# Optimization experiments

Hardware: AMD Instinct MI355X
Metric: run time of the kernel (lower is better)

## Reference

```python
import jax, jax.numpy as jnp
import numpy as np

K = 7            # involution kernel size
GC = 16          # group_channels (canonical involution)
EPS = 1e-6


def ln_cf(x, w, b):
    # channels_first LayerNorm over channel dim (axis=1), as in ConvNeXt utils
    u = jnp.mean(x, axis=1, keepdims=True)
    s = jnp.mean((x - u) ** 2, axis=1, keepdims=True)
    xn = (x - u) / jnp.sqrt(s + EPS)
    return w[:, None, None] * xn + b[:, None, None]


def gelu(x):
    return jax.nn.gelu(x, approximate=False)  # torch nn.GELU default (erf)


def involution(x, w1, b1, w2, b2):
    # x: (B,C,H,W). Kernel-generating head: 1x1 conv -> ReLU -> 1x1 conv.
    B, C, H, W = x.shape
    G = C // GC
    mid = jnp.einsum('bchw,mc->bmhw', x, w1) + b1[None, :, None, None]
    mid = jax.nn.relu(mid)
    wk = jnp.einsum('bmhw,km->bkhw', mid, w2) + b2[None, :, None, None]
    wk = wk.reshape(B, G, K * K, H, W)  # per-pixel, per-group K*K kernels
    pad = (K - 1) // 2
    xp = jnp.pad(x, ((0, 0), (0, 0), (pad, pad), (pad, pad)))
    out = jnp.zeros((B, G, GC, H, W), dtype=x.dtype)
    # accumulate over the K*K spatial offsets (fixed small loop, no big unfold)
    for idx in range(K * K):
        i, j = divmod(idx, K)
        xs = xp[:, :, i:i + H, j:j + W].reshape(B, G, GC, H, W)
        out = out + wk[:, :, idx][:, :, None] * xs
    return out.reshape(B, C, H, W)


def setup_inputs() -> dict:
    key = jax.random.key(0)
    ks = jax.random.split(key, 8)
    B, C, O, H, Wd = 4, 128, 256, 128, 128
    mid = C // 4
    G = C // GC
    sc = 0.05
    return {
        'x': jax.random.normal(ks[0], (B, C, H, Wd), jnp.float32),
        'w1': jax.random.normal(ks[1], (mid, C), jnp.float32) * sc,
        'b1': jnp.zeros((mid,), jnp.float32),
        'w2': jax.random.normal(ks[2], (K * K * G, mid), jnp.float32) * sc,
        'b2': jnp.zeros((K * K * G,), jnp.float32),
        'ln1_w': jnp.ones((C,), jnp.float32),
        'ln1_b': jnp.zeros((C,), jnp.float32),
        'conv_w': jax.random.normal(ks[3], (O, C), jnp.float32) * sc,
        'ln2_w': jnp.ones((O,), jnp.float32),
        'ln2_b': jnp.zeros((O,), jnp.float32),
        'map_w': jax.random.normal(ks[4], (O, C), jnp.float32) * sc,
        'map_b': jnp.zeros((O,), jnp.float32),
        'ln3_w': jnp.ones((O,), jnp.float32),
        'ln3_b': jnp.zeros((O,), jnp.float32),
    }


def reference(x, w1, b1, w2, b2, ln1_w, ln1_b, conv_w, ln2_w, ln2_b,
              map_w, map_b, ln3_w, ln3_b):
    # invblock: Involution -> LayerNorm(channels_first) -> GELU
    x1 = involution(x, w1, b1, w2, b2)
    x1 = gelu(ln_cf(x1, ln1_w, ln1_b))
    # conv_block: 1x1 conv (no bias) -> LayerNorm
    x1 = ln_cf(jnp.einsum('bchw,oc->bohw', x1, conv_w), ln2_w, ln2_b)
    # mapping (channels differ): 1x1 conv (bias) -> LayerNorm
    xm = jnp.einsum('bchw,oc->bohw', x, map_w) + map_b[None, :, None, None]
    xm = ln_cf(xm, ln3_w, ln3_b)
    return gelu(x1 + xm)
```

## Files before the change

### kernel.cpp

```cpp
#include <hip/hip_runtime.h>

typedef unsigned short ushort_t;
typedef unsigned int uint_t;

#define NB 4
#define NC 128
#define NH 128
#define NW 128
#define NPIX 65536
#define NMID 32
#define NKK 49
#define NK 392
#define NKP 400
#define NO 256
#define LN_EPS 1e-6f

typedef __attribute__((ext_vector_type(8))) short short8;
typedef __attribute__((ext_vector_type(4))) float floatx4;

__device__ __forceinline__ float bf2f(ushort_t u) {
    union { uint_t i; float f; } v; v.i = ((uint_t)u) << 16; return v.f;
}
__device__ __forceinline__ float bf2f_lo(uint_t u) {
    union { uint_t i; float f; } v; v.i = u << 16; return v.f;
}
__device__ __forceinline__ float bf2f_hi(uint_t u) {
    union { uint_t i; float f; } v; v.i = u & 0xffff0000u; return v.f;
}
__device__ __forceinline__ ushort_t f2bf(float f) {
    union { float f; uint_t i; } v; v.f = f;
    uint_t x = v.i;
    uint_t r = (x + 0x7FFFu + ((x >> 16) & 1u)) >> 16;
    return (ushort_t)r;
}
__device__ __forceinline__ float gelu_f(float x) {
    return 0.5f * x * (1.0f + erff(x * 0.70710678118654752f));
}
__device__ __forceinline__ float ldin(const void* p, int i, int isf32) {
    return isf32 ? ((const float*)p)[i] : bf2f(((const ushort_t*)p)[i]);
}
__device__ __forceinline__ void gload_lds16(const void* g, void* l) {
    __builtin_amdgcn_global_load_lds(
        (const __attribute__((address_space(1))) void*)g,
        (__attribute__((address_space(3))) void*)l, 16, 0, 0);
}

__global__ void kdetect(const uint_t* __restrict__ xw, int* __restrict__ flag) {
    int lane = threadIdx.x;
    int cnt = 0;
    for (int j = 0; j < 8; j++) {
        uint_t w = xw[lane * 8 + j];
        uint_t e = (w >> 7) & 0xffu;
        if (e >= 110u && e <= 135u) cnt++;
    }
    for (int d = 1; d < 64; d <<= 1) cnt += __shfl_xor(cnt, d);
    if (lane == 0) flag[0] = (cnt < 256) ? 1 : 0;
}

__global__ void ksentinel(uint_t* __restrict__ out, int nwords) {
    int i = blockIdx.x * 256 + threadIdx.x;
    if (i < nwords) out[i] = 0x40004000u;
}

__global__ __launch_bounds__(256) void ktrans(const void* __restrict__ x,
                                              ushort_t* __restrict__ xT,
                                              const int* __restrict__ flag) {
    int isf32 = flag[0];
    int b = blockIdx.z, h = blockIdx.y;
    int wchunk = blockIdx.x & 1, cchunk = blockIdx.x >> 1;
    int w0 = wchunk << 6, c0 = cchunk << 5;
    __shared__ ushort_t tile[32][66];
    int tx = threadIdx.x & 63, ty = threadIdx.x >> 6;
    for (int r = 0; r < 32; r += 4) {
        int idx = (((b * NC + c0 + r + ty) * NH) + h) * NW + w0 + tx;
        tile[r + ty][tx] = isf32 ? f2bf(((const float*)x)[idx])
                                 : ((const ushort_t*)x)[idx];
    }
    __syncthreads();
    int cc = threadIdx.x & 31, wq = threadIdx.x >> 5;
    for (int pp = 0; pp < 64; pp += 8) {
        int wx = pp + wq;
        xT[((size_t)((b * NH + h) * NW) + w0 + wx) * NC + c0 + cc] = tile[cc][wx];
    }
}

__global__ __launch_bounds__(256) void kprep(const void* w1, const void* w2,
                                             const void* b1, const void* b2,
                                             const void* ln1w, const void* ln1b,
                                             const void* ln2w, const void* ln2b,
                                             const void* map_b,
                                             const void* ln3w, const void* ln3b,
                                             const int* __restrict__ flag,
                                             ushort_t* __restrict__ w1b,
                                             ushort_t* __restrict__ w2b,
                                             float* __restrict__ b1f,
                                             float* __restrict__ b2f,
                                             float* __restrict__ ln1wf,
                                             float* __restrict__ ln1bf,
                                             float* __restrict__ ln2wf,
                                             float* __restrict__ ln2bf,
                                             float* __restrict__ mbf,
                                             float* __restrict__ ln3wf,
                                             float* __restrict__ ln3bf) {
    int isf32 = flag[0];
    int i = blockIdx.x * 256 + threadIdx.x;
    if (i < NMID * NC) w1b[i] = f2bf(ldin(w1, i, isf32));
    if (i < NKP * NMID) w2b[i] = (i < NK * NMID) ? f2bf(ldin(w2, i, isf32))
                                                 : (ushort_t)0;
    if (i < NMID) b1f[i] = ldin(b1, i, isf32);
    if (i < NKP)  b2f[i] = (i < NK) ? ldin(b2, i, isf32) : 0.f;
    if (i < NC) { ln1wf[i] = ldin(ln1w, i, isf32); ln1bf[i] = ldin(ln1b, i, isf32); }
    if (i < NO) {
        ln2wf[i] = ldin(ln2w, i, isf32); ln2bf[i] = ldin(ln2b, i, isf32);
        mbf[i]   = ldin(map_b, i, isf32);
        ln3wf[i] = ldin(ln3w, i, isf32); ln3bf[i] = ldin(ln3b, i, isf32);
    }
}

__global__ __launch_bounds__(256) void kfrag(const void* conv_w, const void* map_w,
                                             const int* __restrict__ flag,
                                             ushort_t* __restrict__ wfrag) {
    int isf32 = flag[0];
    int cid = blockIdx.x * 256 + threadIdx.x;
    int lane = cid & 63, n4 = (cid >> 6) & 15, br = (cid >> 10) & 1, kb = cid >> 11;
    int o = n4 * 16 + (lane & 15);
    int ch0 = kb * 32 + (lane >> 4) * 8;
    const void* src = br ? map_w : conv_w;
    ushort_t* dst = wfrag + (size_t)cid * 8;
#pragma unroll
    for (int j = 0; j < 8; j++)
        dst[j] = f2bf(ldin(src, o * NC + ch0 + j, isf32));
}

__global__ __launch_bounds__(256) void k1a(const ushort_t* __restrict__ xT,
                                           const ushort_t* __restrict__ w1b,
                                           const float* __restrict__ b1f,
                                           const ushort_t* __restrict__ w2b,
                                           const float* __restrict__ b2f,
                                           ushort_t* __restrict__ wkT) {
    __shared__ ushort_t midbuf[64 * 32];
    __shared__ ushort_t wkstage[NKP * 66];

    int t = threadIdx.x;
    int lane = t & 63;
    int w = __builtin_amdgcn_readfirstlane(t >> 6);
    int l16 = lane & 15, quad = lane >> 4;
    int tileid = blockIdx.x;
    int tilex = tileid & 15, tiley = (tileid >> 4) & 15, b = tileid >> 8;
    int h0 = tiley * 8, w0 = tilex * 8;

    int lpx_a = 16 * w + l16;
    int py = lpx_a >> 3, pxx = lpx_a & 7;
    const ushort_t* abase = xT + (size_t)((b * NH + h0 + py) * NW + w0 + pxx) * NC + quad * 8;
    floatx4 am0 = (floatx4)0.f, am1 = (floatx4)0.f;
#pragma unroll
    for (int kb = 0; kb < 4; kb++) {
        short8 a   = *(const short8*)(abase + kb * 32);
        short8 b0  = *(const short8*)(w1b + (l16) * NC + kb * 32 + quad * 8);
        short8 b1v = *(const short8*)(w1b + (16 + l16) * NC + kb * 32 + quad * 8);
        am0 = __builtin_amdgcn_mfma_f32_16x16x32_bf16(a, b0, am0, 0, 0, 0);
        am1 = __builtin_amdgcn_mfma_f32_16x16x32_bf16(a, b1v, am1, 0, 0, 0);
    }
    {
        float bia0 = b1f[l16], bia1 = b1f[16 + l16];
#pragma unroll
        for (int r = 0; r < 4; r++) {
            int m = 16 * w + quad * 4 + r;
            midbuf[m * 32 + l16]      = f2bf(fmaxf(am0[r] + bia0, 0.f));
            midbuf[m * 32 + 16 + l16] = f2bf(fmaxf(am1[r] + bia1, 0.f));
        }
    }
    __syncthreads();

    short8 aM = *(const short8*)(midbuf + (16 * w + l16) * 32 + quad * 8);
#pragma unroll
    for (int nt = 0; nt < 25; nt++) {
        int n = nt * 16 + l16;
        short8 bw = *(const short8*)(w2b + n * 32 + quad * 8);
        floatx4 c = __builtin_amdgcn_mfma_f32_16x16x32_bf16(aM, bw, (floatx4)0.f, 0, 0, 0);
        float bias = b2f[n];
#pragma unroll
        for (int r = 0; r < 4; r++)
            wkstage[n * 66 + 16 * w + quad * 4 + r] = f2bf(c[r] + bias);
    }
    __syncthreads();

    int krow = t >> 5, px2 = t & 31;
    for (int it = 0; it < 50; it++) {
        int k = it * 8 + krow;
        uint_t v = *(const uint_t*)&wkstage[k * 66 + 2 * px2];
        *(uint_t*)&wkT[(size_t)k * NPIX + tileid * 64 + 2 * px2] = v;
    }
}

__global__ __launch_bounds__(512) void k1b(const ushort_t* __restrict__ xT,
                                           const ushort_t* __restrict__ wkT,
                                           const float* __restrict__ ln1wf,
                                           const float* __restrict__ ln1bf,
                                           ushort_t* __restrict__ y1) {
    __shared__ __align__(16) char smem[50432];
    uint4* x8   = (uint4*)smem;
    float* sred = (float*)smem;

    int t = threadIdx.x;
    int lane = t & 63;
    int w = __builtin_amdgcn_readfirstlane(t >> 6);
    int tileid = blockIdx.x;
    int tilex = tileid & 15, tiley = (tileid >> 4) & 15, b = tileid >> 8;
    int h0 = tiley * 8, w0 = tilex * 8;
    int py = lane >> 3, pxx = lane & 7;

    const ushort_t* wkbase = wkT + (size_t)(w * NKK) * NPIX + tileid * 64 + lane;
    uint_t wkp[25];
#pragma unroll
    for (int j = 0; j < 24; j++) {
        uint_t lo = wkbase[(size_t)(2 * j) * NPIX];
        uint_t hi = wkbase[(size_t)(2 * j + 1) * NPIX];
        wkp[j] = lo | (hi << 16);
    }
    wkp[24] = wkbase[(size_t)48 * NPIX];

    for (int it = 0; it < 7; it++) {
        int idx = it * 512 + t;
        if (idx < 3136) {
            int oct = idx & 15, hp = idx >> 4;
            int hy = hp / 14, hx = hp - hy * 14;
            int gh = h0 + hy - 3, gw = w0 + hx - 3;
            uint4 v = make_uint4(0u, 0u, 0u, 0u);
            if ((unsigned)gh < (unsigned)NH && (unsigned)gw < (unsigned)NW) {
                v = *(const uint4*)&xT[(size_t)((b * NH + gh) * NW + gw) * NC + 8 * oct];
            }
            x8[oct * 197 + hp] = v;
        }
    }
    __syncthreads();

    int base0 = py * 14 + pxx;
    float a[16];
#pragma unroll
    for (int j = 0; j < 16; j++) a[j] = 0.f;

#pragma unroll
    for (int tap = 0; tap < NKK; tap++) {
        float wkf = (tap & 1) ? bf2f((ushort_t)(wkp[tap >> 1] >> 16))
                              : bf2f((ushort_t)(wkp[tap >> 1] & 0xffffu));
        int xa = base0 + (tap / 7) * 14 + (tap % 7);
        uint4 u0 = x8[(2 * w) * 197 + xa];
        uint4 u1 = x8[(2 * w + 1) * 197 + xa];
        a[0]  = fmaf(wkf, bf2f_lo(u0.x), a[0]);
        a[1]  = fmaf(wkf, bf2f_hi(u0.x), a[1]);
        a[2]  = fmaf(wkf, bf2f_lo(u0.y), a[2]);
        a[3]  = fmaf(wkf, bf2f_hi(u0.y), a[3]);
        a[4]  = fmaf(wkf, bf2f_lo(u0.z), a[4]);
        a[5]  = fmaf(wkf, bf2f_hi(u0.z), a[5]);
        a[6]  = fmaf(wkf, bf2f_lo(u0.w), a[6]);
        a[7]  = fmaf(wkf, bf2f_hi(u0.w), a[7]);
        a[8]  = fmaf(wkf, bf2f_lo(u1.x), a[8]);
        a[9]  = fmaf(wkf, bf2f_hi(u1.x), a[9]);
        a[10] = fmaf(wkf, bf2f_lo(u1.y), a[10]);
        a[11] = fmaf(wkf, bf2f_hi(u1.y), a[11]);
        a[12] = fmaf(wkf, bf2f_lo(u1.z), a[12]);
        a[13] = fmaf(wkf, bf2f_hi(u1.z), a[13]);
        a[14] = fmaf(wkf, bf2f_lo(u1.w), a[14]);
        a[15] = fmaf(wkf, bf2f_hi(u1.w), a[15]);
    }
    __syncthreads();

    float s = 0.f, sq = 0.f;
#pragma unroll
    for (int j = 0; j < 16; j++) { s += a[j]; sq += a[j] * a[j]; }
    sred[(w * 64 + lane) * 2]     = s;
    sred[(w * 64 + lane) * 2 + 1] = sq;
    __syncthreads();
    float ts = 0.f, tq = 0.f;
#pragma unroll
    for (int r = 0; r < 8; r++) {
        ts += sred[(r * 64 + lane) * 2];
        tq += sred[(r * 64 + lane) * 2 + 1];
    }
    float mean = ts * (1.0f / NC);
    float var = tq * (1.0f / NC) - mean * mean;
    float rstd = rsqrtf(var + LN_EPS);

    int p = (b * NH + h0 + py) * NW + w0 + pxx;
    uint_t pk[8];
#pragma unroll
    for (int j = 0; j < 8; j++) {
        int c0 = 16 * w + 2 * j;
        float g0 = gelu_f((a[2 * j] - mean) * rstd * ln1wf[c0] + ln1bf[c0]);
        float g1 = gelu_f((a[2 * j + 1] - mean) * rstd * ln1wf[c0 + 1] + ln1bf[c0 + 1]);
        pk[j] = (uint_t)f2bf(g0) | ((uint_t)f2bf(g1) << 16);
    }
    uint4* dst = (uint4*)(y1 + (size_t)p * NC + 16 * w);
    dst[0] = make_uint4(pk[0], pk[1], pk[2], pk[3]);
    dst[1] = make_uint4(pk[4], pk[5], pk[6], pk[7]);
}

__global__ __launch_bounds__(64) void k1_fused(const ushort_t* __restrict__ xT,
                                               const ushort_t* __restrict__ w1b,
                                               const float* __restrict__ b1f,
                                               const ushort_t* __restrict__ w2b,
                                               const float* __restrict__ b2f,
                                               const float* __restrict__ ln1wf,
                                               const float* __restrict__ ln1bf,
                                               ushort_t* __restrict__ y1) {
    __shared__ ushort_t midbuf[16 * 32];
    __shared__ ushort_t wkbuf[16 * NKP];

    int lane = threadIdx.x;
    int l16 = lane & 15, quad = lane >> 4;
    int b = blockIdx.z;
    int h0 = blockIdx.y * 2, w0 = blockIdx.x * 8;

    int Pa = (b * NH + h0 + (l16 >> 3)) * NW + w0 + (l16 & 7);
    const ushort_t* abase = xT + (size_t)Pa * NC + quad * 8;
    floatx4 am0 = (floatx4)0.f, am1 = (floatx4)0.f;
#pragma unroll
    for (int kb = 0; kb < 4; kb++) {
        short8 a   = *(const short8*)(abase + kb * 32);
        short8 b0  = *(const short8*)(w1b + (l16) * NC + kb * 32 + quad * 8);
        short8 b1v = *(const short8*)(w1b + (16 + l16) * NC + kb * 32 + quad * 8);
        am0 = __builtin_amdgcn_mfma_f32_16x16x32_bf16(a, b0, am0, 0, 0, 0);
        am1 = __builtin_amdgcn_mfma_f32_16x16x32_bf16(a, b1v, am1, 0, 0, 0);
    }
    {
        float bia0 = b1f[l16], bia1 = b1f[16 + l16];
#pragma unroll
        for (int r = 0; r < 4; r++) {
            int m = quad * 4 + r;
            midbuf[m * 32 + l16]      = f2bf(fmaxf(am0[r] + bia0, 0.f));
            midbuf[m * 32 + 16 + l16] = f2bf(fmaxf(am1[r] + bia1, 0.f));
        }
    }
    __syncthreads();

    short8 aM = *(const short8*)(midbuf + l16 * 32 + quad * 8);
#pragma unroll
    for (int nt = 0; nt < 25; nt++) {
        int n = nt * 16 + l16;
        short8 bw = *(const short8*)(w2b + n * 32 + quad * 8);
        floatx4 c = __builtin_amdgcn_mfma_f32_16x16x32_bf16(aM, bw, (floatx4)0.f, 0, 0, 0);
        float bias = b2f[n];
#pragma unroll
        for (int r = 0; r < 4; r++)
            wkbuf[(quad * 4 + r) * NKP + n] = f2bf(c[r] + bias);
    }
    __syncthreads();

    int g = lane >> 3;
    float l1w0 = ln1wf[2 * lane], l1w1 = ln1wf[2 * lane + 1];
    float l1b0 = ln1bf[2 * lane], l1b1 = ln1bf[2 * lane + 1];

    for (int i = 0; i < 16; i++) {
        int hh0 = h0 + (i >> 3), ww0 = w0 + (i & 7);
        int p = (b * NH + hh0) * NW + ww0;
        const ushort_t* wkrow = wkbuf + i * NKP + g * NKK;
        float a0 = 0.f, a1 = 0.f;
#pragma unroll
        for (int dy = -3; dy <= 3; dy++) {
            int hh = hh0 + dy;
            if ((unsigned)hh >= (unsigned)NH) continue;
#pragma unroll
            for (int dx = -3; dx <= 3; dx++) {
                int ww = ww0 + dx;
                if ((unsigned)ww >= (unsigned)NW) continue;
                float wkv = bf2f(wkrow[(dy + 3) * 7 + (dx + 3)]);
                uint_t xp = *(const uint_t*)(xT + ((size_t)(p + dy * NW + dx)) * NC + 2 * lane);
                a0 = fmaf(wkv, bf2f((ushort_t)(xp & 0xffffu)), a0);
                a1 = fmaf(wkv, bf2f((ushort_t)(xp >> 16)), a1);
            }
        }
        float s = a0 + a1, sq = a0 * a0 + a1 * a1;
#pragma unroll
        for (int d = 1; d < 64; d <<= 1) {
            s  += __shfl_xor(s, d);
            sq += __shfl_xor(sq, d);
        }
        float mean = s * (1.0f / NC);
        float var = sq * (1.0f / NC) - mean * mean;
        float rstd = rsqrtf(var + LN_EPS);
        float g0 = gelu_f((a0 - mean) * rstd * l1w0 + l1b0);
        float g1 = gelu_f((a1 - mean) * rstd * l1w1 + l1b1);
        uint_t pk = (uint_t)f2bf(g0) | ((uint_t)f2bf(g1) << 16);
        *(uint_t*)(y1 + (size_t)p * NC + 2 * lane) = pk;
    }
}

__global__ __launch_bounds__(256, 2) void k23(const ushort_t* __restrict__ y1,
                                              const ushort_t* __restrict__ xT,
                                              const ushort_t* __restrict__ wfrag,
                                              const float* __restrict__ mbf,
                                              const float* __restrict__ ln2wf,
                                              const float* __restrict__ ln2bf,
                                              const float* __restrict__ ln3wf,
                                              const float* __restrict__ ln3bf,
                                              void* __restrict__ out,
                                              const int* __restrict__ flag) {
    __shared__ __align__(16) char sbuf[65536];

    int isf32 = flag[0];
    int t = threadIdx.x;
    int lane = t & 63;
    int w = __builtin_amdgcn_readfirstlane(t >> 6);
    int quad = lane >> 4, l16 = lane & 15;

    int P0 = blockIdx.x * 64;
    int pw = P0 + w * 16;
    const ushort_t* aYp = y1 + (size_t)(pw + l16) * NC + quad * 8;
    const ushort_t* aXp = xT + (size_t)(pw + l16) * NC + quad * 8;

    {
        const ushort_t* gsrc = wfrag + (size_t)(w * 512 + lane) * 8;
        char* ldst = sbuf + (size_t)(w * 512) * 16;
#pragma unroll
        for (int i = 0; i < 8; i++)
            gload_lds16(gsrc + i * 64 * 8, ldst + i * 64 * 16);
    }
    short8 aYr[4], aXr[4];
#pragma unroll
    for (int kb = 0; kb < 4; kb++) {
        aYr[kb] = *(const short8*)(aYp + kb * 32);
        aXr[kb] = *(const short8*)(aXp + kb * 32);
    }
    __syncthreads();

    floatx4 accC[16], accM[16];
#pragma unroll
    for (int n4 = 0; n4 < 16; n4++) { accC[n4] = (floatx4)0.f; accM[n4] = (floatx4)0.f; }

#pragma unroll
    for (int kb = 0; kb < 4; kb++) {
        const char* bufr = sbuf + (kb & 1) * 32768;
        if (kb < 3) {
            char* bufw = sbuf + ((kb + 1) & 1) * 32768;
            const ushort_t* gsrc = wfrag + ((size_t)(kb + 1) * 2048 + w * 512 + lane) * 8;
            char* ldst = bufw + (size_t)(w * 512) * 16;
#pragma unroll
            for (int i = 0; i < 8; i++)
                gload_lds16(gsrc + i * 64 * 8, ldst + i * 64 * 16);
        }
        short8 aY = aYr[kb], aX = aXr[kb];
#pragma unroll
        for (int n4 = 0; n4 < 16; n4++) {
            short8 bc = *(const short8*)(bufr + (size_t)(n4 * 64 + lane) * 16);
            short8 bm = *(const short8*)(bufr + (size_t)(1024 + n4 * 64 + lane) * 16);
            accC[n4] = __builtin_amdgcn_mfma_f32_16x16x32_bf16(aY, bc, accC[n4], 0, 0, 0);
            accM[n4] = __builtin_amdgcn_mfma_f32_16x16x32_bf16(aX, bm, accM[n4], 0, 0, 0);
        }
        if (kb < 3) __syncthreads();
    }

#pragma unroll
    for (int n4 = 0; n4 < 16; n4++) {
        float mb = mbf[n4 * 16 + l16];
#pragma unroll
        for (int r = 0; r < 4; r++) accM[n4][r] += mb;
    }

    floatx4 s1 = (floatx4)0.f, q1 = (floatx4)0.f, s2 = (floatx4)0.f, q2 = (floatx4)0.f;
#pragma unroll
    for (int n4 = 0; n4 < 16; n4++)
#pragma unroll
        for (int r = 0; r < 4; r++) {
            float a = accC[n4][r], m = accM[n4][r];
            s1[r] += a; q1[r] += a * a;
            s2[r] += m; q2[r] += m * m;
        }
#pragma unroll
    for (int d = 1; d < 16; d <<= 1) {
#pragma unroll
        for (int r = 0; r < 4; r++) {
            s1[r] += __shfl_xor(s1[r], d);
            q1[r] += __shfl_xor(q1[r], d);
            s2[r] += __shfl_xor(s2[r], d);
            q2[r] += __shfl_xor(q2[r], d);
        }
    }
    floatx4 m1, r1, m2, r2;
#pragma unroll
    for (int r = 0; r < 4; r++) {
        m1[r] = s1[r] * (1.0f / NO);
        r1[r] = rsqrtf(q1[r] * (1.0f / NO) - m1[r] * m1[r] + LN_EPS);
        m2[r] = s2[r] * (1.0f / NO);
        r2[r] = rsqrtf(q2[r] * (1.0f / NO) - m2[r] * m2[r] + LN_EPS);
    }

    int batch = pw >> 14;
    int plocal = (pw & 16383) + quad * 4;
#pragma unroll
    for (int n4 = 0; n4 < 16; n4++) {
        int o = n4 * 16 + l16;
        float l2w = ln2wf[o], l2b = ln2bf[o];
        float l3w = ln3wf[o], l3b = ln3bf[o];
        float4 gv;
        {
            float v1, v2;
            v1 = (accC[n4][0] - m1[0]) * r1[0] * l2w + l2b;
            v2 = (accM[n4][0] - m2[0]) * r2[0] * l3w + l3b;
            gv.x = gelu_f(v1 + v2);
            v1 = (accC[n4][1] - m1[1]) * r1[1] * l2w + l2b;
            v2 = (accM[n4][1] - m2[1]) * r2[1] * l3w + l3b;
            gv.y = gelu_f(v1 + v2);
            v1 = (accC[n4][2] - m1[2]) * r1[2] * l2w + l2b;
            v2 = (accM[n4][2] - m2[2]) * r2[2] * l3w + l3b;
            gv.z = gelu_f(v1 + v2);
            v1 = (accC[n4][3] - m1[3]) * r1[3] * l2w + l2b;
            v2 = (accM[n4][3] - m2[3]) * r2[3] * l3w + l3b;
            gv.w = gelu_f(v1 + v2);
        }
        size_t oi = ((size_t)(batch * NO + o) << 14) + plocal;
        if (isf32) {
            *(float4*)((float*)out + oi) = gv;
        } else {
            uint_t p0 = (uint_t)f2bf(gv.x) | ((uint_t)f2bf(gv.y) << 16);
            uint_t p1 = (uint_t)f2bf(gv.z) | ((uint_t)f2bf(gv.w) << 16);
            *(uint2*)((ushort_t*)out + oi) = make_uint2(p0, p1);
        }
    }
}

extern "C" void kernel_launch(void* const* d_in, const int* in_sizes, int n_in,
                              void* d_out, int out_size, void* d_ws, size_t ws_size,
                              hipStream_t stream) {
    const void* x      = d_in[0];
    const void* w1     = d_in[1];
    const void* b1     = d_in[2];
    const void* w2     = d_in[3];
    const void* b2     = d_in[4];
    const void* ln1w   = d_in[5];
    const void* ln1b   = d_in[6];
    const void* conv_w = d_in[7];
    const void* ln2w   = d_in[8];
    const void* ln2b   = d_in[9];
    const void* map_w  = d_in[10];
    const void* map_b  = d_in[11];
    const void* ln3w   = d_in[12];
    const void* ln3b   = d_in[13];

    char* ws = (char*)d_ws;
    ushort_t* xT    = (ushort_t*)(ws);
    ushort_t* y1    = (ushort_t*)(ws + 16777216);
    ushort_t* wfrag = (ushort_t*)(ws + 33554432);
    ushort_t* w1b   = (ushort_t*)(ws + 33685504);
    ushort_t* w2b   = (ushort_t*)(ws + 33693696);
    float*    b1f   = (float*)(ws + 33719296);
    float*    b2f   = (float*)(ws + 33719424);
    float*    ln1wf = (float*)(ws + 33721024);
    float*    ln1bf = (float*)(ws + 33721536);
    float*    mbf   = (float*)(ws + 33722048);
    float*    ln2wf = (float*)(ws + 33723072);
    float*    ln2bf = (float*)(ws + 33724096);
    float*    ln3wf = (float*)(ws + 33725120);
    float*    ln3bf = (float*)(ws + 33726144);
    int*      flag  = (int*)(ws + 33727168);
    const size_t NEED_SMALL = 33727184;
    ushort_t* wkT   = (ushort_t*)(ws + 33727232);
    const size_t NEED_BIG = 33727232 + (size_t)NKP * NPIX * 2;

    if (ws_size < NEED_SMALL) {
        int nwords = out_size / 2;
        ksentinel<<<(nwords + 255) / 256, 256, 0, stream>>>((uint_t*)d_out, nwords);
        return;
    }

    kdetect<<<1, 64, 0, stream>>>((const uint_t*)x, flag);
    kprep<<<128, 256, 0, stream>>>(w1, w2, b1, b2, ln1w, ln1b,
                                   ln2w, ln2b, map_b, ln3w, ln3b, flag,
                                   w1b, w2b, b1f, b2f, ln1wf, ln1bf,
                                   ln2wf, ln2bf, mbf, ln3wf, ln3bf);
    kfrag<<<32, 256, 0, stream>>>(conv_w, map_w, flag, wfrag);
    ktrans<<<dim3(8, 128, 4), 256, 0, stream>>>(x, xT, flag);

    if (ws_size >= NEED_BIG) {
        k1a<<<1024, 256, 0, stream>>>(xT, w1b, b1f, w2b, b2f, wkT);
        k1b<<<1024, 512, 0, stream>>>(xT, wkT, ln1wf, ln1bf, y1);
    } else {
        k1_fused<<<dim3(16, 64, 4), 64, 0, stream>>>(xT, w1b, b1f, w2b, b2f,
                                                     ln1wf, ln1bf, y1);
    }

    k23<<<NPIX / 64, 256, 0, stream>>>(y1, xT, wfrag, mbf,
                                       ln2wf, ln2bf, ln3wf, ln3bf, d_out, flag);
}
```

Before: 229.9 us.

## Split k23 conv and mapping GEMMs across wave pairs to raise occupancy

k23 now pairs waves: one wave of each pair computes the conv GEMM plus LN2 for 16 pixels, the other computes the mapping GEMM plus LN3. The two halves are exchanged through shared memory before the final add and GELU. Each wave keeps half the accumulators, LDS drops to 32KB with single buffering, launch bounds go to 4 blocks per CU, and the grid doubles to 32 pixels per block. This is meant to cut register and LDS pressure and raise occupancy. The cost is losing the double-buffered weight prefetch, which adds an extra barrier per k-step, plus an extra LDS exchange.

```diff
diff --git a/kernel.cpp b/kernel.cpp
--- a/kernel.cpp
+++ b/kernel.cpp
@@ -386,7 +386,7 @@
     }
 }
 
-__global__ __launch_bounds__(256, 2) void k23(const ushort_t* __restrict__ y1,
+__global__ __launch_bounds__(256, 4) void k23(const ushort_t* __restrict__ y1,
                                               const ushort_t* __restrict__ xT,
                                               const ushort_t* __restrict__ wfrag,
                                               const float* __restrict__ mbf,
@@ -396,18 +396,19 @@
                                               const float* __restrict__ ln3bf,
                                               void* __restrict__ out,
                                               const int* __restrict__ flag) {
-    __shared__ __align__(16) char sbuf[65536];
+    __shared__ __align__(16) char sbuf[32768];
 
     int isf32 = flag[0];
     int t = threadIdx.x;
     int lane = t & 63;
     int w = __builtin_amdgcn_readfirstlane(t >> 6);
     int quad = lane >> 4, l16 = lane & 15;
-
-    int P0 = blockIdx.x * 64;
-    int pw = P0 + w * 16;
-    const ushort_t* aYp = y1 + (size_t)(pw + l16) * NC + quad * 8;
-    const ushort_t* aXp = xT + (size_t)(pw + l16) * NC + quad * 8;
+    int pair = w >> 1;
+    int isM  = w & 1;
+
+    int P0 = blockIdx.x * 32;
+    int pw = P0 + pair * 16;
+    const ushort_t* Abase = (isM ? xT : y1) + (size_t)(pw + l16) * NC + quad * 8;
 
     {
         const ushort_t* gsrc = wfrag + (size_t)(w * 512 + lane) * 8;
@@ -416,104 +417,110 @@
         for (int i = 0; i < 8; i++)
             gload_lds16(gsrc + i * 64 * 8, ldst + i * 64 * 16);
     }
-    short8 aYr[4], aXr[4];
+    short8 Ar[4];
+#pragma unroll
+    for (int kb = 0; kb < 4; kb++) Ar[kb] = *(const short8*)(Abase + kb * 32);
+
+    __syncthreads();
+
+    floatx4 acc[16];
+#pragma unroll
+    for (int n4 = 0; n4 < 16; n4++) acc[n4] = (floatx4)0.f;
+
+    const char* bbase = sbuf + isM * 16384;
 #pragma unroll
     for (int kb = 0; kb < 4; kb++) {
-        aYr[kb] = *(const short8*)(aYp + kb * 32);
-        aXr[kb] = *(const short8*)(aXp + kb * 32);
-    }
-    __syncthreads();
-
-    floatx4 accC[16], accM[16];
-#pragma unroll
-    for (int n4 = 0; n4 < 16; n4++) { accC[n4] = (floatx4)0.f; accM[n4] = (floatx4)0.f; }
-
-#pragma unroll
-    for (int kb = 0; kb < 4; kb++) {
-        const char* bufr = sbuf + (kb & 1) * 32768;
+        short8 a = Ar[kb];
+#pragma unroll
+        for (int n4 = 0; n4 < 16; n4++) {
+            short8 b = *(const short8*)(bbase + (size_t)(n4 * 64 + lane) * 16);
+            acc[n4] = __builtin_amdgcn_mfma_f32_16x16x32_bf16(a, b, acc[n4], 0, 0, 0);
+        }
+        __syncthreads();
         if (kb < 3) {
-            char* bufw = sbuf + ((kb + 1) & 1) * 32768;
             const ushort_t* gsrc = wfrag + ((size_t)(kb + 1) * 2048 + w * 512 + lane) * 8;
-            char* ldst = bufw + (size_t)(w * 512) * 16;
+            char* ldst = sbuf + (size_t)(w * 512) * 16;
 #pragma unroll
             for (int i = 0; i < 8; i++)
                 gload_lds16(gsrc + i * 64 * 8, ldst + i * 64 * 16);
-        }
-        short8 aY = aYr[kb], aX = aXr[kb];
+            __syncthreads();
+        }
+    }
+
+    if (isM) {
 #pragma unroll
         for (int n4 = 0; n4 < 16; n4++) {
-            short8 bc = *(const short8*)(bufr + (size_t)(n4 * 64 + lane) * 16);
-            short8 bm = *(const short8*)(bufr + (size_t)(1024 + n4 * 64 + lane) * 16);
-            accC[n4] = __builtin_amdgcn_mfma_f32_16x16x32_bf16(aY, bc, accC[n4], 0, 0, 0);
-            accM[n4] = __builtin_amdgcn_mfma_f32_16x16x32_bf16(aX, bm, accM[n4], 0, 0, 0);
-        }
-        if (kb < 3) __syncthreads();
-    }
-
+            float mb = mbf[n4 * 16 + l16];
+#pragma unroll
+            for (int r = 0; r < 4; r++) acc[n4][r] += mb;
+        }
+    }
+
+    floatx4 s = (floatx4)0.f, q = (floatx4)0.f;
+#pragma unroll
+    for (int n4 = 0; n4 < 16; n4++)
+#pragma unroll
+        for (int r = 0; r < 4; r++) {
+            float a = acc[n4][r];
+            s[r] += a; q[r] += a * a;
+        }
+#pragma unroll
+    for (int d = 1; d < 16; d <<= 1) {
+#pragma unroll
+        for (int r = 0; r < 4; r++) {
+            s[r] += __shfl_xor(s[r], d);
+            q[r] += __shfl_xor(q[r], d);
+        }
+    }
+    floatx4 mn, rs;
+#pragma unroll
+    for (int r = 0; r < 4; r++) {
+        mn[r] = s[r] * (1.0f / NO);
+        rs[r] = rsqrtf(q[r] * (1.0f / NO) - mn[r] * mn[r] + LN_EPS);
+    }
+
+    const float* lnw = isM ? ln3wf : ln2wf;
+    const float* lnb = isM ? ln3bf : ln2bf;
 #pragma unroll
     for (int n4 = 0; n4 < 16; n4++) {
-        float mb = mbf[n4 * 16 + l16];
-#pragma unroll
-        for (int r = 0; r < 4; r++) accM[n4][r] += mb;
-    }
-
-    floatx4 s1 = (floatx4)0.f, q1 = (floatx4)0.f, s2 = (floatx4)0.f, q2 = (floatx4)0.f;
-#pragma unroll
-    for (int n4 = 0; n4 < 16; n4++)
-#pragma unroll
-        for (int r = 0; r < 4; r++) {
-            float a = accC[n4][r], m = accM[n4][r];
-            s1[r] += a; q1[r] += a * a;
-            s2[r] += m; q2[r] += m * m;
-        }
-#pragma unroll
-    for (int d = 1; d < 16; d <<= 1) {
-#pragma unroll
-        for (int r = 0; r < 4; r++) {
-            s1[r] += __shfl_xor(s1[r], d);
-            q1[r] += __shfl_xor(q1[r], d);
-            s2[r] += __shfl_xor(s2[r], d);
-            q2[r] += __shfl_xor(q2[r], d);
-        }
-    }
-    floatx4 m1, r1, m2, r2;
-#pragma unroll
-    for (int r = 0; r < 4; r++) {
-        m1[r] = s1[r] * (1.0f / NO);
-        r1[r] = rsqrtf(q1[r] * (1.0f / NO) - m1[r] * m1[r] + LN_EPS);
-        m2[r] = s2[r] * (1.0f / NO);
-        r2[r] = rsqrtf(q2[r] * (1.0f / NO) - m2[r] * m2[r] + LN_EPS);
-    }
-
+        int o = n4 * 16 + l16;
+        float ww = lnw[o], bb = lnb[o];
+#pragma unroll
+        for (int r = 0; r < 4; r++)
+            acc[n4][r] = (acc[n4][r] - mn[r]) * rs[r] * ww + bb;
+    }
+
+    float* preg = (float*)(sbuf + pair * 16384);
+    if (!isM) {
+#pragma unroll
+        for (int j = 0; j < 8; j++)
+            *(floatx4*)(preg + j * 256 + lane * 4) = acc[8 + j];
+    } else {
+#pragma unroll
+        for (int j = 0; j < 8; j++)
+            *(floatx4*)(preg + 2048 + j * 256 + lane * 4) = acc[j];
+    }
+    __syncthreads();
+
+    int n4base = isM ? 8 : 0;
+    const float* rdp = preg + (isM ? 0 : 2048);
     int batch = pw >> 14;
     int plocal = (pw & 16383) + quad * 4;
 #pragma unroll
-    for (int n4 = 0; n4 < 16; n4++) {
+    for (int j = 0; j < 8; j++) {
+        int n4 = n4base + j;
+        floatx4 other = *(const floatx4*)(rdp + j * 256 + lane * 4);
+        float g0 = gelu_f(acc[n4][0] + other[0]);
+        float g1 = gelu_f(acc[n4][1] + other[1]);
+        float g2 = gelu_f(acc[n4][2] + other[2]);
+        float g3 = gelu_f(acc[n4][3] + other[3]);
         int o = n4 * 16 + l16;
-        float l2w = ln2wf[o], l2b = ln2bf[o];
-        float l3w = ln3wf[o], l3b = ln3bf[o];
-        float4 gv;
-        {
-            float v1, v2;
-            v1 = (accC[n4][0] - m1[0]) * r1[0] * l2w + l2b;
-            v2 = (accM[n4][0] - m2[0]) * r2[0] * l3w + l3b;
-            gv.x = gelu_f(v1 + v2);
-            v1 = (accC[n4][1] - m1[1]) * r1[1] * l2w + l2b;
-            v2 = (accM[n4][1] - m2[1]) * r2[1] * l3w + l3b;
-            gv.y = gelu_f(v1 + v2);
-            v1 = (accC[n4][2] - m1[2]) * r1[2] * l2w + l2b;
-            v2 = (accM[n4][2] - m2[2]) * r2[2] * l3w + l3b;
-            gv.z = gelu_f(v1 + v2);
-            v1 = (accC[n4][3] - m1[3]) * r1[3] * l2w + l2b;
-            v2 = (accM[n4][3] - m2[3]) * r2[3] * l3w + l3b;
-            gv.w = gelu_f(v1 + v2);
-        }
         size_t oi = ((size_t)(batch * NO + o) << 14) + plocal;
         if (isf32) {
-            *(float4*)((float*)out + oi) = gv;
+            *(float4*)((float*)out + oi) = make_float4(g0, g1, g2, g3);
         } else {
-            uint_t p0 = (uint_t)f2bf(gv.x) | ((uint_t)f2bf(gv.y) << 16);
-            uint_t p1 = (uint_t)f2bf(gv.z) | ((uint_t)f2bf(gv.w) << 16);
+            uint_t p0 = (uint_t)f2bf(g0) | ((uint_t)f2bf(g1) << 16);
+            uint_t p1 = (uint_t)f2bf(g2) | ((uint_t)f2bf(g3) << 16);
             *(uint2*)((ushort_t*)out + oi) = make_uint2(p0, p1);
         }
     }
@@ -579,6 +586,6 @@
                                                      ln1wf, ln1bf, y1);
     }
 
-    k23<<<NPIX / 64, 256, 0, stream>>>(y1, xT, wfrag, mbf,
+    k23<<<NPIX / 32, 256, 0, stream>>>(y1, xT, wfrag, mbf,
                                        ln2wf, ln2bf, ln3wf, ln3bf, d_out, flag);
 }
```

Result: slower. 331.8 us (+44.4%).

## Split k23 output channels across wave pairs and single-buffer weight LDS

Applied to the files above, without the earlier changes.

Each 16-pixel tile in k23 is now shared by two waves, and each wave computes half of the 256 output channels. The two halves' LayerNorm partial sums are combined through shared memory. This halves the accumulator registers per wave. The weight staging buffer goes from double to single buffering (32KB), and launch bounds rise to 3 blocks per CU. The aim is higher occupancy and more blocks, in exchange for losing the overlap of weight loads with MFMA, adding extra barriers, and loading each A fragment redundantly in both waves of a pair.

```diff
diff --git a/kernel.cpp b/kernel.cpp
--- a/kernel.cpp
+++ b/kernel.cpp
@@ -386,7 +386,7 @@
     }
 }
 
-__global__ __launch_bounds__(256, 2) void k23(const ushort_t* __restrict__ y1,
+__global__ __launch_bounds__(256, 3) void k23(const ushort_t* __restrict__ y1,
                                               const ushort_t* __restrict__ xT,
                                               const ushort_t* __restrict__ wfrag,
                                               const float* __restrict__ mbf,
@@ -396,16 +396,18 @@
                                               const float* __restrict__ ln3bf,
                                               void* __restrict__ out,
                                               const int* __restrict__ flag) {
-    __shared__ __align__(16) char sbuf[65536];
+    __shared__ __align__(16) char sbuf[32768];
 
     int isf32 = flag[0];
     int t = threadIdx.x;
     int lane = t & 63;
     int w = __builtin_amdgcn_readfirstlane(t >> 6);
     int quad = lane >> 4, l16 = lane & 15;
-
-    int P0 = blockIdx.x * 64;
-    int pw = P0 + w * 16;
+    int pair = w >> 1;
+    int oh   = w & 1;
+
+    int P0 = blockIdx.x * 32;
+    int pw = P0 + pair * 16;
     const ushort_t* aYp = y1 + (size_t)(pw + l16) * NC + quad * 8;
     const ushort_t* aXp = xT + (size_t)(pw + l16) * NC + quad * 8;
 
@@ -416,53 +418,53 @@
         for (int i = 0; i < 8; i++)
             gload_lds16(gsrc + i * 64 * 8, ldst + i * 64 * 16);
     }
-    short8 aYr[4], aXr[4];
+    short8 Ay[4], Ax[4];
 #pragma unroll
     for (int kb = 0; kb < 4; kb++) {
-        aYr[kb] = *(const short8*)(aYp + kb * 32);
-        aXr[kb] = *(const short8*)(aXp + kb * 32);
-    }
-    __syncthreads();
-
-    floatx4 accC[16], accM[16];
-#pragma unroll
-    for (int n4 = 0; n4 < 16; n4++) { accC[n4] = (floatx4)0.f; accM[n4] = (floatx4)0.f; }
+        Ay[kb] = *(const short8*)(aYp + kb * 32);
+        Ax[kb] = *(const short8*)(aXp + kb * 32);
+    }
+    __syncthreads();
+
+    floatx4 accC[8], accM[8];
+#pragma unroll
+    for (int j = 0; j < 8; j++) { accC[j] = (floatx4)0.f; accM[j] = (floatx4)0.f; }
 
 #pragma unroll
     for (int kb = 0; kb < 4; kb++) {
-        const char* bufr = sbuf + (kb & 1) * 32768;
+        short8 ay = Ay[kb], ax = Ax[kb];
+#pragma unroll
+        for (int j = 0; j < 8; j++) {
+            int n4 = oh * 8 + j;
+            short8 bc = *(const short8*)(sbuf + (size_t)(n4 * 64 + lane) * 16);
+            short8 bm = *(const short8*)(sbuf + 16384 + (size_t)(n4 * 64 + lane) * 16);
+            accC[j] = __builtin_amdgcn_mfma_f32_16x16x32_bf16(ay, bc, accC[j], 0, 0, 0);
+            accM[j] = __builtin_amdgcn_mfma_f32_16x16x32_bf16(ax, bm, accM[j], 0, 0, 0);
+        }
+        __syncthreads();
         if (kb < 3) {
-            char* bufw = sbuf + ((kb + 1) & 1) * 32768;
             const ushort_t* gsrc = wfrag + ((size_t)(kb + 1) * 2048 + w * 512 + lane) * 8;
-            char* ldst = bufw + (size_t)(w * 512) * 16;
+            char* ldst = sbuf + (size_t)(w * 512) * 16;
 #pragma unroll
             for (int i = 0; i < 8; i++)
                 gload_lds16(gsrc + i * 64 * 8, ldst + i * 64 * 16);
-        }
-        short8 aY = aYr[kb], aX = aXr[kb];
-#pragma unroll
-        for (int n4 = 0; n4 < 16; n4++) {
-            short8 bc = *(const short8*)(bufr + (size_t)(n4 * 64 + lane) * 16);
-            short8 bm = *(const short8*)(bufr + (size_t)(1024 + n4 * 64 + lane) * 16);
-            accC[n4] = __builtin_amdgcn_mfma_f32_16x16x32_bf16(aY, bc, accC[n4], 0, 0, 0);
-            accM[n4] = __builtin_amdgcn_mfma_f32_16x16x32_bf16(aX, bm, accM[n4], 0, 0, 0);
-        }
-        if (kb < 3) __syncthreads();
-    }
-
-#pragma unroll
-    for (int n4 = 0; n4 < 16; n4++) {
-        float mb = mbf[n4 * 16 + l16];
-#pragma unroll
-        for (int r = 0; r < 4; r++) accM[n4][r] += mb;
+            __syncthreads();
+        }
+    }
+
+#pragma unroll
+    for (int j = 0; j < 8; j++) {
+        float mb = mbf[(oh * 8 + j) * 16 + l16];
+#pragma unroll
+        for (int r = 0; r < 4; r++) accM[j][r] += mb;
     }
 
     floatx4 s1 = (floatx4)0.f, q1 = (floatx4)0.f, s2 = (floatx4)0.f, q2 = (floatx4)0.f;
 #pragma unroll
-    for (int n4 = 0; n4 < 16; n4++)
+    for (int j = 0; j < 8; j++)
 #pragma unroll
         for (int r = 0; r < 4; r++) {
-            float a = accC[n4][r], m = accM[n4][r];
+            float a = accC[j][r], m = accM[j][r];
             s1[r] += a; q1[r] += a * a;
             s2[r] += m; q2[r] += m * m;
         }
@@ -476,36 +478,50 @@
             q2[r] += __shfl_xor(q2[r], d);
         }
     }
-    floatx4 m1, r1, m2, r2;
+
+    float* sstat = (float*)sbuf;
+    if (l16 == 0) {
+#pragma unroll
+        for (int r = 0; r < 4; r++) {
+            float* sp = sstat + (((pair * 2 + oh) * 16) + quad * 4 + r) * 4;
+            sp[0] = s1[r]; sp[1] = q1[r]; sp[2] = s2[r]; sp[3] = q2[r];
+        }
+    }
+    __syncthreads();
+
+    floatx4 mn1, rs1, mn2, rs2;
 #pragma unroll
     for (int r = 0; r < 4; r++) {
-        m1[r] = s1[r] * (1.0f / NO);
-        r1[r] = rsqrtf(q1[r] * (1.0f / NO) - m1[r] * m1[r] + LN_EPS);
-        m2[r] = s2[r] * (1.0f / NO);
-        r2[r] = rsqrtf(q2[r] * (1.0f / NO) - m2[r] * m2[r] + LN_EPS);
+        const float* op = sstat + (((pair * 2 + (oh ^ 1)) * 16) + quad * 4 + r) * 4;
+        float S1 = s1[r] + op[0], Q1 = q1[r] + op[1];
+        float S2 = s2[r] + op[2], Q2 = q2[r] + op[3];
+        mn1[r] = S1 * (1.0f / NO);
+        rs1[r] = rsqrtf(Q1 * (1.0f / NO) - mn1[r] * mn1[r] + LN_EPS);
+        mn2[r] = S2 * (1.0f / NO);
+        rs2[r] = rsqrtf(Q2 * (1.0f / NO) - mn2[r] * mn2[r] + LN_EPS);
     }
 
     int batch = pw >> 14;
     int plocal = (pw & 16383) + quad * 4;
 #pragma unroll
-    for (int n4 = 0; n4 < 16; n4++) {
-        int o = n4 * 16 + l16;
+    for (int j = 0; j < 8; j++) {
+        int o = (oh * 8 + j) * 16 + l16;
         float l2w = ln2wf[o], l2b = ln2bf[o];
         float l3w = ln3wf[o], l3b = ln3bf[o];
         float4 gv;
         {
             float v1, v2;
-            v1 = (accC[n4][0] - m1[0]) * r1[0] * l2w + l2b;
-            v2 = (accM[n4][0] - m2[0]) * r2[0] * l3w + l3b;
+            v1 = (accC[j][0] - mn1[0]) * rs1[0] * l2w + l2b;
+            v2 = (accM[j][0] - mn2[0]) * rs2[0] * l3w + l3b;
             gv.x = gelu_f(v1 + v2);
-            v1 = (accC[n4][1] - m1[1]) * r1[1] * l2w + l2b;
-            v2 = (accM[n4][1] - m2[1]) * r2[1] * l3w + l3b;
+            v1 = (accC[j][1] - mn1[1]) * rs1[1] * l2w + l2b;
+            v2 = (accM[j][1] - mn2[1]) * rs2[1] * l3w + l3b;
             gv.y = gelu_f(v1 + v2);
-            v1 = (accC[n4][2] - m1[2]) * r1[2] * l2w + l2b;
-            v2 = (accM[n4][2] - m2[2]) * r2[2] * l3w + l3b;
+            v1 = (accC[j][2] - mn1[2]) * rs1[2] * l2w + l2b;
+            v2 = (accM[j][2] - mn2[2]) * rs2[2] * l3w + l3b;
             gv.z = gelu_f(v1 + v2);
-            v1 = (accC[n4][3] - m1[3]) * r1[3] * l2w + l2b;
-            v2 = (accM[n4][3] - m2[3]) * r2[3] * l3w + l3b;
+            v1 = (accC[j][3] - mn1[3]) * rs1[3] * l2w + l2b;
+            v2 = (accM[j][3] - mn2[3]) * rs2[3] * l3w + l3b;
             gv.w = gelu_f(v1 + v2);
         }
         size_t oi = ((size_t)(batch * NO + o) << 14) + plocal;
@@ -579,6 +595,6 @@
                                                      ln1wf, ln1bf, y1);
     }
 
-    k23<<<NPIX / 64, 256, 0, stream>>>(y1, xT, wfrag, mbf,
+    k23<<<NPIX / 32, 256, 0, stream>>>(y1, xT, wfrag, mbf,
                                        ln2wf, ln2bf, ln3wf, ln3bf, d_out, flag);
 }
```

Result: no change. 228.5 us (-0.6%).
